# Kernel optimization log

Measured on AMD Instinct MI355X. Metric: run time of the kernel, lower is better.

## Reference

```python
import jax, jax.numpy as jnp
import numpy as np
import math

B, S, DIM = 32, 1, 4096          # decode: batch 32, one new token
HQ, HKV, HD = 32, 8, 128         # GQA: 32 query heads, 8 kv heads, head_dim 128
MAXS = 2048                      # cache capacity
START = 2047                     # attend over the full 2048-token cache


def _rope(x, cos, sin):
    # x: [B, S, H, D]; pairs (x[2i], x[2i+1]) rotated by angle theta -> complex multiply
    p = x.reshape(*x.shape[:-1], HD // 2, 2)
    xr, xi = p[..., 0], p[..., 1]
    c = cos[None, :, None, :]    # [1, S, 1, D/2]
    s = sin[None, :, None, :]
    out_r = xr * c - xi * s
    out_i = xr * s + xi * c
    return jnp.stack([out_r, out_i], axis=-1).reshape(x.shape)


def setup_inputs() -> dict:
    key = jax.random.key(0)
    ks = jax.random.split(key, 8)
    x = jax.random.normal(ks[0], (B, S, DIM), jnp.float32)
    scale = 0.02
    wq = jax.random.normal(ks[1], (HQ * HD, DIM), jnp.float32) * scale
    wk = jax.random.normal(ks[2], (HKV * HD, DIM), jnp.float32) * scale
    wv = jax.random.normal(ks[3], (HKV * HD, DIM), jnp.float32) * scale
    wo = jax.random.normal(ks[4], (DIM, HQ * HD), jnp.float32) * scale
    k_cache = jax.random.normal(ks[5], (B, MAXS, HKV, HD), jnp.float32)
    v_cache = jax.random.normal(ks[6], (B, MAXS, HKV, HD), jnp.float32)
    # true rotary angles for positions [START, START+S)
    pos = jnp.arange(START, START + S, dtype=jnp.float32)
    inv_freq = 1.0 / (10000.0 ** (jnp.arange(0, HD, 2, dtype=jnp.float32) / HD))
    ang = pos[:, None] * inv_freq[None, :]           # [S, HD/2]
    return {
        "x": x,
        "freqs_cos": jnp.cos(ang),
        "freqs_sin": jnp.sin(ang),
        "wq": wq, "wk": wk, "wv": wv, "wo": wo,
        "k_cache": k_cache, "v_cache": v_cache,
        "start_pos": START,
    }


def reference(x, freqs_cos, freqs_sin, wq, wk, wv, wo, k_cache, v_cache, start_pos):
    b, s, _ = x.shape
    xq = (x @ wq.T).reshape(b, s, HQ, HD)
    xk = (x @ wk.T).reshape(b, s, HKV, HD)
    xv = (x @ wv.T).reshape(b, s, HKV, HD)
    xq = _rope(xq, freqs_cos, freqs_sin)
    xk = _rope(xk, freqs_cos, freqs_sin)
    # KV-cache update (start_pos is a static Python int)
    k_cache = k_cache.at[:, start_pos:start_pos + s].set(xk)
    v_cache = v_cache.at[:, start_pos:start_pos + s].set(xv)
    keys = k_cache[:, :start_pos + s]     # [B, T, HKV, HD]
    values = v_cache[:, :start_pos + s]
    rep = HQ // HKV
    q = xq.reshape(b, s, HKV, rep, HD)
    # grouped attention -- equivalent to repeat_kv without materializing expanded K/V
    scores = jnp.einsum('bsgrd,btgd->bgrst', q, keys) / math.sqrt(HD)
    probs = jax.nn.softmax(scores.astype(jnp.float32), axis=-1).astype(x.dtype)
    out = jnp.einsum('bgrst,btgd->bsgrd', probs, values).reshape(b, s, HQ * HD)
    return out @ wo.T
```

## Files before the change

kernel.cpp:

```cpp
#include <hip/hip_runtime.h>

#define NB   32
#define DIM  4096
#define HQ   32
#define HKV  8
#define HD   128
#define MAXS 2048

#define TSPLIT 4
#define CH   (MAXS / TSPLIT)

__global__ __launch_bounds__(256)
void gemv32(const float* __restrict__ W, const float* __restrict__ X,
            float* __restrict__ C, int K, long strideB)
{
    __shared__ __align__(16) float xs[32][68];
    __shared__ __align__(16) float wt[64][68];
    const int tid = threadIdx.x;
    const int bg  = tid & 7;
    const int mg  = tid >> 3;
    const int row0 = blockIdx.x * 64;
    const int ks   = K / gridDim.y;
    const int kbeg = blockIdx.y * ks;
    const int kend = kbeg + ks;

    float acc[2][4] = {};

    for (int k0 = kbeg; k0 < kend; k0 += 64) {
        for (int i = tid; i < 32 * 16; i += 256) {
            int b = i >> 4, kq = i & 15;
            float4 v = *(const float4*)(X + (long)b * K + k0 + kq * 4);
            *(float4*)&xs[b][kq * 4] = v;
        }
        for (int i = tid; i < 64 * 16; i += 256) {
            int m = i >> 4, kq = i & 15;
            float4 v = *(const float4*)(W + (long)(row0 + m) * K + k0 + kq * 4);
            *(float4*)&wt[m][kq * 4] = v;
        }
        __syncthreads();
        #pragma unroll
        for (int kq = 0; kq < 16; ++kq) {
            float4 w0 = *(const float4*)&wt[mg * 2 + 0][kq * 4];
            float4 w1 = *(const float4*)&wt[mg * 2 + 1][kq * 4];
            #pragma unroll
            for (int j = 0; j < 4; ++j) {
                float4 xv = *(const float4*)&xs[bg + 8 * j][kq * 4];
                acc[0][j] = fmaf(w0.x, xv.x, acc[0][j]);
                acc[0][j] = fmaf(w0.y, xv.y, acc[0][j]);
                acc[0][j] = fmaf(w0.z, xv.z, acc[0][j]);
                acc[0][j] = fmaf(w0.w, xv.w, acc[0][j]);
                acc[1][j] = fmaf(w1.x, xv.x, acc[1][j]);
                acc[1][j] = fmaf(w1.y, xv.y, acc[1][j]);
                acc[1][j] = fmaf(w1.z, xv.z, acc[1][j]);
                acc[1][j] = fmaf(w1.w, xv.w, acc[1][j]);
            }
        }
        __syncthreads();
    }
    #pragma unroll
    for (int j = 0; j < 4; ++j) {
        int b = bg + 8 * j;
        atomicAdd(&C[(long)b * strideB + row0 + mg * 2 + 0], acc[0][j]);
        atomicAdd(&C[(long)b * strideB + row0 + mg * 2 + 1], acc[1][j]);
    }
}

__global__ __launch_bounds__(256)
void rope_scatter(float* __restrict__ q_buf, const float* __restrict__ k_new,
                  const float* __restrict__ v_new, float* __restrict__ k_cache,
                  float* __restrict__ v_cache, const float* __restrict__ fc,
                  const float* __restrict__ fs, const int* __restrict__ sp)
{
    const int start = sp[0];
    const int gt = blockIdx.x * 256 + threadIdx.x;
    const int NT = gridDim.x * 256;

    for (int i = gt; i < NB * HQ * 64; i += NT) {
        int b = i >> 11, r = i & 2047, p = r & 63;
        float c = fc[p], s = fs[p];
        float2 xv = *(float2*)(q_buf + (long)b * DIM + 2 * r);
        float2 ov = make_float2(xv.x * c - xv.y * s, xv.x * s + xv.y * c);
        *(float2*)(q_buf + (long)b * DIM + 2 * r) = ov;
    }
    for (int i = gt; i < NB * HKV * 64; i += NT) {
        int b = i >> 9, r = i & 511, p = r & 63;
        float c = fc[p], s = fs[p];
        float2 xv = *(const float2*)(k_new + (long)b * (HKV * HD) + 2 * r);
        float2 ov = make_float2(xv.x * c - xv.y * s, xv.x * s + xv.y * c);
        *(float2*)(k_cache + ((long)b * MAXS + start) * (HKV * HD) + 2 * r) = ov;
    }
    for (int i = gt; i < NB * HKV * HD / 4; i += NT) {
        int b = i >> 8, j = i & 255;
        float4 v = *(const float4*)(v_new + (long)b * (HKV * HD) + 4 * j);
        *(float4*)(v_cache + ((long)b * MAXS + start) * (HKV * HD) + 4 * j) = v;
    }
}

__global__ __launch_bounds__(512)
void attention_part(const float* __restrict__ q_buf,
                    const float* __restrict__ k_cache,
                    const float* __restrict__ v_cache,
                    float* __restrict__ part_o,
                    float2* __restrict__ part_ml,
                    const int* __restrict__ sp)
{
    const int g = blockIdx.x, b = blockIdx.y, ts = blockIdx.z;
    const int tid = threadIdx.x;
    const int wave = tid >> 6, lane = tid & 63;
    const int L = sp[0] + 1;
    const int tbeg = ts * CH;

    __shared__ __align__(16) float qs[4 * HD];
    __shared__ __align__(16) float sc[4][CH];
    __shared__ __align__(16) float outred[16 * HD];
    __shared__ float wred[8];
    __shared__ float m_sh[4], l_sh[4];

    for (int i = tid; i < 4 * HD; i += 512)
        qs[i] = q_buf[(long)b * DIM + g * 4 * HD + i];
    __syncthreads();

    const float scale = 0.08838834764831845f;
    const float* Kbase = k_cache + ((long)b * MAXS * HKV + g) * HD;

    {
        const int r = lane & 3, tr = lane >> 2;
        #pragma unroll
        for (int grp = 0; grp < CH / 128; ++grp) {
            int tl = wave * (CH / 8) + grp * 16 + tr;
            int t  = tbeg + tl;
            const float* Kt = Kbase + (long)t * (HKV * HD);
            float a0 = 0.f, a1 = 0.f;
            #pragma unroll
            for (int kq = 0; kq < 16; ++kq) {
                float4 kv = *(const float4*)(Kt + kq * 4);
                float4 qv = *(const float4*)(qs + r * HD + kq * 4);
                a0 = fmaf(kv.x, qv.x, a0);
                a0 = fmaf(kv.y, qv.y, a0);
                a0 = fmaf(kv.z, qv.z, a0);
                a0 = fmaf(kv.w, qv.w, a0);
            }
            #pragma unroll
            for (int kq = 16; kq < 32; ++kq) {
                float4 kv = *(const float4*)(Kt + kq * 4);
                float4 qv = *(const float4*)(qs + r * HD + kq * 4);
                a1 = fmaf(kv.x, qv.x, a1);
                a1 = fmaf(kv.y, qv.y, a1);
                a1 = fmaf(kv.z, qv.z, a1);
                a1 = fmaf(kv.w, qv.w, a1);
            }
            sc[r][tl] = (t < L) ? (a0 + a1) * scale : -3.0e38f;
        }
    }
    __syncthreads();

    const int h = tid >> 7, idx = tid & 127;
    {
        float mx = -3.0e38f;
        for (int tl = idx; tl < CH; tl += 128) mx = fmaxf(mx, sc[h][tl]);
        #pragma unroll
        for (int o = 32; o > 0; o >>= 1) mx = fmaxf(mx, __shfl_xor(mx, o, 64));
        if (lane == 0) wred[wave] = mx;
        __syncthreads();
        if (tid < 4) m_sh[tid] = fmaxf(wred[2 * tid], wred[2 * tid + 1]);
        __syncthreads();
        float m = m_sh[h];
        float ssum = 0.f;
        for (int tl = idx; tl < CH; tl += 128) {
            float sv = sc[h][tl];
            float p = (sv > -1.0e37f) ? __expf(sv - m) : 0.f;
            sc[h][tl] = p;
            ssum += p;
        }
        #pragma unroll
        for (int o = 32; o > 0; o >>= 1) ssum += __shfl_xor(ssum, o, 64);
        if (lane == 0) wred[wave] = ssum;
        __syncthreads();
        if (tid < 4) l_sh[tid] = wred[2 * tid] + wred[2 * tid + 1];
        __syncthreads();
    }

    {
        const int hp = tid >> 7;
        const int tc = (tid >> 5) & 3;
        const int dq = tid & 31;
        const float* Vb = v_cache + ((long)b * MAXS * HKV + g) * HD + dq * 4;
        float4 a = make_float4(0.f, 0.f, 0.f, 0.f);
        const int tl0 = tc * (CH / 4);
        #pragma unroll 8
        for (int i = 0; i < CH / 4; ++i) {
            int tl = tl0 + i;
            float p = sc[hp][tl];
            float4 v = *(const float4*)(Vb + (long)(tbeg + tl) * (HKV * HD));
            a.x = fmaf(p, v.x, a.x);
            a.y = fmaf(p, v.y, a.y);
            a.z = fmaf(p, v.z, a.z);
            a.w = fmaf(p, v.w, a.w);
        }
        *(float4*)&outred[(hp * 4 + tc) * HD + dq * 4] = a;
    }
    __syncthreads();
    {
        const int d = tid & 127;
        float o = outred[(h * 4 + 0) * HD + d] + outred[(h * 4 + 1) * HD + d]
                + outred[(h * 4 + 2) * HD + d] + outred[(h * 4 + 3) * HD + d];
        long po = ((((long)b * HKV + g) * TSPLIT + ts) * 4 + h) * HD + d;
        part_o[po] = o;
        if (d == 0)
            part_ml[(((long)b * HKV + g) * TSPLIT + ts) * 4 + h] =
                make_float2(m_sh[h], l_sh[h]);
    }
}

__global__ __launch_bounds__(512)
void attention_combine(const float* __restrict__ part_o,
                       const float2* __restrict__ part_ml,
                       float* __restrict__ attn)
{
    const int g = blockIdx.x, b = blockIdx.y;
    const int h = threadIdx.x >> 7, d = threadIdx.x & 127;
    const float2* ml = part_ml + ((long)b * HKV + g) * TSPLIT * 4 + h;
    float M = -3.0e38f;
    #pragma unroll
    for (int ts = 0; ts < TSPLIT; ++ts) M = fmaxf(M, ml[ts * 4].x);
    const float* po = part_o + (((long)b * HKV + g) * TSPLIT * 4 + h) * HD + d;
    float num = 0.f, denom = 0.f;
    #pragma unroll
    for (int ts = 0; ts < TSPLIT; ++ts) {
        float2 mlv = ml[ts * 4];
        float w = (mlv.x > -1.0e37f) ? __expf(mlv.x - M) : 0.f;
        denom += mlv.y * w;
        num   += po[(long)ts * 4 * HD] * w;
    }
    attn[(long)b * DIM + g * 4 * HD + h * HD + d] = num / denom;
}

extern "C" void kernel_launch(void* const* d_in, const int* in_sizes, int n_in,
                              void* d_out, int out_size, void* d_ws, size_t ws_size,
                              hipStream_t stream)
{
    const float* x    = (const float*)d_in[0];
    const float* fcos = (const float*)d_in[1];
    const float* fsin = (const float*)d_in[2];
    const float* wq   = (const float*)d_in[3];
    const float* wk   = (const float*)d_in[4];
    const float* wv   = (const float*)d_in[5];
    const float* wo   = (const float*)d_in[6];
    float* k_cache    = (float*)d_in[7];
    float* v_cache    = (float*)d_in[8];
    const int* sp     = (const int*)d_in[9];
    float* out        = (float*)d_out;

    float* q_buf = (float*)d_ws;
    float* k_new = q_buf + NB * DIM;
    float* v_new = k_new + NB * HKV * HD;
    float* attn  = v_new + NB * HKV * HD;
    float* part_o = attn + NB * DIM;
    float2* part_ml = (float2*)(part_o + (long)NB * HKV * TSPLIT * 4 * HD);

    hipMemsetAsync(d_ws, 0, (size_t)(NB * DIM + 2 * NB * HKV * HD) * 4, stream);
    hipMemsetAsync(d_out, 0, (size_t)NB * DIM * 4, stream);

    gemv32<<<dim3(64, 8), 256, 0, stream>>>(wq, x, q_buf, DIM, DIM);
    gemv32<<<dim3(16, 16), 256, 0, stream>>>(wk, x, k_new, DIM, HKV * HD);
    gemv32<<<dim3(16, 16), 256, 0, stream>>>(wv, x, v_new, DIM, HKV * HD);
    rope_scatter<<<256, 256, 0, stream>>>(q_buf, k_new, v_new, k_cache, v_cache,
                                          fcos, fsin, sp);
    attention_part<<<dim3(HKV, NB, TSPLIT), 512, 0, stream>>>(
        q_buf, k_cache, v_cache, part_o, part_ml, sp);
    attention_combine<<<dim3(HKV, NB), 512, 0, stream>>>(part_o, part_ml, attn);
    gemv32<<<dim3(64, 8), 256, 0, stream>>>(wo, attn, out, DIM, DIM);
}
```

Baseline: 851.3 us.

## Stream GEMV operands directly from global; tile K through LDS in attention scores

The projection GEMV drops its shared-memory staging and barriers. Each thread now reads its two weight rows and four activation rows straight from global memory with float4 loads, relying on cache for reuse across threads. The attention score phase keeps q in registers and stages 32-token K tiles into LDS. Four lanes then split each head-dim dot product and combine partial sums with shuffles, which gives coalesced K loads. This adds 16 barrier-separated tile iterations and reuses the K tile buffer for the output reduction.

Measured after the change: 940.9 us. +10.5%, slower.

```diff
diff --git a/kernel.cpp b/kernel.cpp
--- a/kernel.cpp
+++ b/kernel.cpp
@@ -10,53 +10,48 @@
 #define TSPLIT 4
 #define CH   (MAXS / TSPLIT)
 
+__device__ inline void fma4(float& a, float4 w, float4 x)
+{
+    a = fmaf(w.x, x.x, a);
+    a = fmaf(w.y, x.y, a);
+    a = fmaf(w.z, x.z, a);
+    a = fmaf(w.w, x.w, a);
+}
+
 __global__ __launch_bounds__(256)
 void gemv32(const float* __restrict__ W, const float* __restrict__ X,
             float* __restrict__ C, int K, long strideB)
 {
-    __shared__ __align__(16) float xs[32][68];
-    __shared__ __align__(16) float wt[64][68];
     const int tid = threadIdx.x;
     const int bg  = tid & 7;
     const int mg  = tid >> 3;
     const int row0 = blockIdx.x * 64;
     const int ks   = K / gridDim.y;
     const int kbeg = blockIdx.y * ks;
-    const int kend = kbeg + ks;
+
+    const float* wp0 = W + (long)(row0 + 2 * mg) * K + kbeg;
+    const float* wp1 = wp0 + K;
+    const float* xp0 = X + (long)(bg +  0) * K + kbeg;
+    const float* xp1 = X + (long)(bg +  8) * K + kbeg;
+    const float* xp2 = X + (long)(bg + 16) * K + kbeg;
+    const float* xp3 = X + (long)(bg + 24) * K + kbeg;
 
     float acc[2][4] = {};
 
-    for (int k0 = kbeg; k0 < kend; k0 += 64) {
-        for (int i = tid; i < 32 * 16; i += 256) {
-            int b = i >> 4, kq = i & 15;
-            float4 v = *(const float4*)(X + (long)b * K + k0 + kq * 4);
-            *(float4*)&xs[b][kq * 4] = v;
-        }
-        for (int i = tid; i < 64 * 16; i += 256) {
-            int m = i >> 4, kq = i & 15;
-            float4 v = *(const float4*)(W + (long)(row0 + m) * K + k0 + kq * 4);
-            *(float4*)&wt[m][kq * 4] = v;
-        }
-        __syncthreads();
-        #pragma unroll
-        for (int kq = 0; kq < 16; ++kq) {
-            float4 w0 = *(const float4*)&wt[mg * 2 + 0][kq * 4];
-            float4 w1 = *(const float4*)&wt[mg * 2 + 1][kq * 4];
-            #pragma unroll
-            for (int j = 0; j < 4; ++j) {
-                float4 xv = *(const float4*)&xs[bg + 8 * j][kq * 4];
-                acc[0][j] = fmaf(w0.x, xv.x, acc[0][j]);
-                acc[0][j] = fmaf(w0.y, xv.y, acc[0][j]);
-                acc[0][j] = fmaf(w0.z, xv.z, acc[0][j]);
-                acc[0][j] = fmaf(w0.w, xv.w, acc[0][j]);
-                acc[1][j] = fmaf(w1.x, xv.x, acc[1][j]);
-                acc[1][j] = fmaf(w1.y, xv.y, acc[1][j]);
-                acc[1][j] = fmaf(w1.z, xv.z, acc[1][j]);
-                acc[1][j] = fmaf(w1.w, xv.w, acc[1][j]);
-            }
-        }
-        __syncthreads();
-    }
+    #pragma unroll 4
+    for (int k = 0; k < ks; k += 4) {
+        float4 w0 = *(const float4*)(wp0 + k);
+        float4 w1 = *(const float4*)(wp1 + k);
+        float4 x0 = *(const float4*)(xp0 + k);
+        float4 x1 = *(const float4*)(xp1 + k);
+        float4 x2 = *(const float4*)(xp2 + k);
+        float4 x3 = *(const float4*)(xp3 + k);
+        fma4(acc[0][0], w0, x0);  fma4(acc[1][0], w1, x0);
+        fma4(acc[0][1], w0, x1);  fma4(acc[1][1], w1, x1);
+        fma4(acc[0][2], w0, x2);  fma4(acc[1][2], w1, x2);
+        fma4(acc[0][3], w0, x3);  fma4(acc[1][3], w1, x3);
+    }
+
     #pragma unroll
     for (int j = 0; j < 4; ++j) {
         int b = bg + 8 * j;
@@ -110,54 +105,52 @@
     const int L = sp[0] + 1;
     const int tbeg = ts * CH;
 
-    __shared__ __align__(16) float qs[4 * HD];
-    __shared__ __align__(16) float sc[4][CH];
-    __shared__ __align__(16) float outred[16 * HD];
+    __shared__ __align__(16) float kt[32][132];
+    __shared__ __align__(16) float sc_s[4][CH];
     __shared__ float wred[8];
     __shared__ float m_sh[4], l_sh[4];
-
-    for (int i = tid; i < 4 * HD; i += 512)
-        qs[i] = q_buf[(long)b * DIM + g * 4 * HD + i];
-    __syncthreads();
+    float* outred = &kt[0][0];
 
     const float scale = 0.08838834764831845f;
     const float* Kbase = k_cache + ((long)b * MAXS * HKV + g) * HD;
 
-    {
-        const int r = lane & 3, tr = lane >> 2;
-        #pragma unroll
-        for (int grp = 0; grp < CH / 128; ++grp) {
-            int tl = wave * (CH / 8) + grp * 16 + tr;
-            int t  = tbeg + tl;
-            const float* Kt = Kbase + (long)t * (HKV * HD);
-            float a0 = 0.f, a1 = 0.f;
-            #pragma unroll
-            for (int kq = 0; kq < 16; ++kq) {
-                float4 kv = *(const float4*)(Kt + kq * 4);
-                float4 qv = *(const float4*)(qs + r * HD + kq * 4);
-                a0 = fmaf(kv.x, qv.x, a0);
-                a0 = fmaf(kv.y, qv.y, a0);
-                a0 = fmaf(kv.z, qv.z, a0);
-                a0 = fmaf(kv.w, qv.w, a0);
-            }
-            #pragma unroll
-            for (int kq = 16; kq < 32; ++kq) {
-                float4 kv = *(const float4*)(Kt + kq * 4);
-                float4 qv = *(const float4*)(qs + r * HD + kq * 4);
-                a1 = fmaf(kv.x, qv.x, a1);
-                a1 = fmaf(kv.y, qv.y, a1);
-                a1 = fmaf(kv.z, qv.z, a1);
-                a1 = fmaf(kv.w, qv.w, a1);
-            }
-            sc[r][tl] = (t < L) ? (a0 + a1) * scale : -3.0e38f;
-        }
-    }
-    __syncthreads();
+    const int r  = tid >> 4;
+    const int hh = (tid >> 2) & 3;
+    const int e  = tid & 3;
+    float4 qreg[8];
+    {
+        const float* qsrc = q_buf + (long)b * DIM + g * 4 * HD + hh * HD + e * 32;
+        #pragma unroll
+        for (int c = 0; c < 8; ++c) qreg[c] = *(const float4*)(qsrc + c * 4);
+    }
+
+    for (int tile = 0; tile < 16; ++tile) {
+        const int base_t = tbeg + tile * 32;
+        for (int i = tid; i < 32 * 32; i += 512) {
+            int row = i >> 5, c4 = i & 31;
+            *(float4*)&kt[row][c4 * 4] =
+                *(const float4*)(Kbase + (long)(base_t + row) * (HKV * HD) + c4 * 4);
+        }
+        __syncthreads();
+        float a = 0.f;
+        #pragma unroll
+        for (int c = 0; c < 8; ++c) {
+            float4 kv = *(const float4*)&kt[r][e * 32 + c * 4];
+            fma4(a, kv, qreg[c]);
+        }
+        a += __shfl_xor(a, 1, 64);
+        a += __shfl_xor(a, 2, 64);
+        if (e == 0) {
+            int t = base_t + r;
+            sc_s[hh][tile * 32 + r] = (t < L) ? a * scale : -3.0e38f;
+        }
+        __syncthreads();
+    }
 
     const int h = tid >> 7, idx = tid & 127;
     {
         float mx = -3.0e38f;
-        for (int tl = idx; tl < CH; tl += 128) mx = fmaxf(mx, sc[h][tl]);
+        for (int tl = idx; tl < CH; tl += 128) mx = fmaxf(mx, sc_s[h][tl]);
         #pragma unroll
         for (int o = 32; o > 0; o >>= 1) mx = fmaxf(mx, __shfl_xor(mx, o, 64));
         if (lane == 0) wred[wave] = mx;
@@ -167,9 +160,9 @@
         float m = m_sh[h];
         float ssum = 0.f;
         for (int tl = idx; tl < CH; tl += 128) {
-            float sv = sc[h][tl];
+            float sv = sc_s[h][tl];
             float p = (sv > -1.0e37f) ? __expf(sv - m) : 0.f;
-            sc[h][tl] = p;
+            sc_s[h][tl] = p;
             ssum += p;
         }
         #pragma unroll
@@ -190,7 +183,7 @@
         #pragma unroll 8
         for (int i = 0; i < CH / 4; ++i) {
             int tl = tl0 + i;
-            float p = sc[hp][tl];
+            float p = sc_s[hp][tl];
             float4 v = *(const float4*)(Vb + (long)(tbeg + tl) * (HKV * HD));
             a.x = fmaf(p, v.x, a.x);
             a.y = fmaf(p, v.y, a.y);
```
